# Kernel tuning notes

Measured on AMD Instinct MI355X. Metric: run time of the kernel, lower is better.

The kernel has to match this reference:

```python
import jax, jax.numpy as jnp
import jax.lax as lax
import numpy as np

# ---- Parallel3DGeometry constants ----
B, C = 1, 1
D, H, W = 64, 96, 96          # internal volume layout (z, y, x)
V, U, A = 64, 96, 90          # detector rows, detector cols, projection angles
SX = SY = SD = 1.0            # voxel size (x, y, z)
SU = SV = 1.0                 # detector spacing
NSTEPS = H + W + 2            # upper bound on voxels crossed by an XY ray
DIAG = float(np.sqrt(SX * SX + SY * SY))
EPS = 1e-12


def _t_for(p0, dp, pmin, pmax):
    # slab entry/exit parameters, matching torch _t_for (incl. parallel-ray cases)
    par = jnp.abs(dp) < EPS
    safe = jnp.where(par, 1.0, dp)
    t0 = (pmin - p0) / safe
    t1 = (pmax - p0) / safe
    lo = jnp.minimum(t0, t1)
    hi = jnp.maximum(t0, t1)
    inside = (p0 >= pmin) & (p0 <= pmax)
    lo = jnp.where(par, jnp.where(inside, -jnp.inf, jnp.inf), lo)
    hi = jnp.where(par, jnp.where(inside, jnp.inf, -jnp.inf), hi)
    return lo, hi


def _trace():
    """Vectorized Siddon XY traversal for all A*U rays.

    Returns Is, Js (int32 [A,U,NSTEPS]) voxel indices and Ws (f32 [A,U,NSTEPS])
    segment lengths (0 where the ray has exited / padded steps).
    """
    angles = jnp.linspace(0.0, np.pi, A, endpoint=False).astype(jnp.float32)
    cos_t = jnp.cos(angles)
    sin_t = jnp.sin(angles)
    u = (jnp.arange(U, dtype=jnp.float32) - (U - 1) / 2.0) * SU
    dx = jnp.broadcast_to(cos_t[:, None], (A, U)).reshape(-1)
    dy = jnp.broadcast_to(sin_t[:, None], (A, U)).reshape(-1)
    x0 = (-u[None, :] * sin_t[:, None]).reshape(-1)
    y0 = (u[None, :] * cos_t[:, None]).reshape(-1)

    x_min = -((W - 1) / 2.0) * SX; x_max = ((W - 1) / 2.0) * SX
    y_min = -((H - 1) / 2.0) * SY; y_max = ((H - 1) / 2.0) * SY
    tx0, tx1 = _t_for(x0, dx, x_min, x_max)
    ty0, ty1 = _t_for(y0, dy, y_min, y_max)
    t_entry = jnp.maximum(tx0, ty0)
    t_exit = jnp.minimum(tx1, ty1)
    alive0 = t_entry < t_exit
    te = jnp.where(alive0, t_entry, 0.0)
    tex = jnp.where(alive0, t_exit, 0.0)
    xe = x0 + te * dx
    ye = y0 + te * dy
    i0 = jnp.clip(jnp.round(xe / SX + (W - 1) / 2.0), 0, W - 1).astype(jnp.int32)
    j0 = jnp.clip(jnp.round(ye / SY + (H - 1) / 2.0), 0, H - 1).astype(jnp.int32)
    cxw = (W - 1) / 2.0 * SX
    cyh = (H - 1) / 2.0 * SY

    def body(st, _):
        i, j, x, y, t, alive = st
        valid = alive & (t < tex - EPS)
        fi = i.astype(jnp.float32)
        fj = j.astype(jnp.float32)
        xn = jnp.where(dx > 0, (fi + 0.5) * SX - cxw,
                       jnp.where(dx < 0, (fi - 0.5) * SX - cxw, jnp.inf))
        yn = jnp.where(dy > 0, (fj + 0.5) * SY - cyh,
                       jnp.where(dy < 0, (fj - 0.5) * SY - cyh, jnp.inf))
        okx = jnp.abs(dx) > EPS
        oky = jnp.abs(dy) > EPS
        tx = jnp.where(okx, (xn - x) / jnp.where(okx, dx, 1.0), jnp.inf)
        ty = jnp.where(oky, (yn - y) / jnp.where(oky, dy, 1.0), jnp.inf)
        dt = jnp.minimum(jnp.minimum(tx, ty), tex - t)
        seg = jnp.maximum(0.0, dt * DIAG / jnp.maximum(jnp.abs(dx) + jnp.abs(dy), EPS))
        w = jnp.where(valid, seg, 0.0)
        i_n = i + jnp.where(tx <= ty, jnp.where(dx > 0, 1, -1), 0)
        j_n = j + jnp.where(ty <= tx, jnp.where(dy > 0, 1, -1), 0)
        inb = (i_n >= 0) & (i_n < W) & (j_n >= 0) & (j_n < H)
        dts = jnp.where(valid, dt, 0.0)
        st2 = (jnp.where(valid, i_n, i), jnp.where(valid, j_n, j),
               x + dx * dts, y + dy * dts, t + dts, valid & inb)
        return st2, (i, j, w)

    init = (i0, j0, xe, ye, te, alive0)
    _, (Is, Js, Ws) = lax.scan(body, init, None, length=NSTEPS)
    # [NSTEPS, R] -> [A, U, NSTEPS]
    Is = Is.T.reshape(A, U, NSTEPS)
    Js = Js.T.reshape(A, U, NSTEPS)
    Ws = Ws.T.reshape(A, U, NSTEPS)
    return Is, Js, Ws


def _forward(vol):
    # model-facing [B,C,X,Y,Z] -> internal [B,C,D,H,W]
    vol_int = jnp.transpose(vol, (0, 1, 4, 3, 2))
    Is, Js, Ws = _trace()
    v_phys = (jnp.arange(V, dtype=jnp.float32) - (V - 1) / 2.0) * SV
    k = jnp.clip(jnp.round(v_phys / SD + (D - 1) / 2.0), 0, D - 1).astype(jnp.int32)
    # gather voxel values along every ray: [B,C,V,A,U,NSTEPS]
    g = vol_int[:, :, k[:, None, None, None], Js[None], Is[None]]
    out = jnp.einsum('bcvaun,aun->bcvau', g, Ws.astype(vol.dtype))
    # internal [B,C,V,A,U] (== out[b,c,a,v,u] reordered) -> model-facing [B,C,U,A,V]
    return jnp.transpose(out, (0, 1, 4, 3, 2))


def setup_inputs() -> dict:
    key = jax.random.key(0)
    vol = jax.random.normal(key, (B, C, W, H, D), dtype=jnp.float32)
    return {"vol": vol}


def reference(vol):
    return _forward(vol)
```

## Files before the change

### kernel.cpp

```cpp
#include <hip/hip_runtime.h>
#include <math.h>

namespace {
constexpr int NA = 90, NU = 96, NV = 64, NW = 96, NH = 96, ND = 64;
constexpr int NRAY   = NA * NU;
constexpr int NVOX   = NW * NH * ND;
constexpr int NENT   = 256;
constexpr int CNTMAX = 208;
constexpr int TILE   = 8;
constexpr int NBLK   = 1024;
constexpr int NEXTRA = NRAY - NBLK * TILE;
}

__device__ inline void sincos_poly(double xd, float* s, float* c)
{
    const double INV_PIO2 = 0.63661977236758134308;
    const double PIO2_HI  = 1.57079632679489655800e+00;
    const double PIO2_LO  = 6.12323399573676603587e-17;
    const double qd = rint(xd * INV_PIO2);
    const double r  = (xd - qd * PIO2_HI) - qd * PIO2_LO;
    const double z  = r * r;
    const double sp = r + (r * z) * (-1.66666666666666324348e-01 + z *
                     ( 8.33333333332248946124e-03 + z *
                     (-1.98412698298579493134e-04 + z *
                     ( 2.75573137070700676789e-06 + z *
                     (-2.50507602534068634195e-08 + z *
                       1.58969099521155010221e-10)))));
    const double cp = 1.0 + z * (-0.5 + z *
                     ( 4.16666666666666019037e-02 + z *
                     (-1.38888888888741095749e-03 + z *
                     ( 2.48015872894767294178e-05 + z *
                     (-2.75573143513906633035e-07 + z *
                     ( 2.08757232129817482790e-09 + z *
                      -1.13596475577881948265e-11))))));
    const int q = (int)qd;
    const double sv = (q == 0) ? sp : ((q == 1) ? cp : -sp);
    const double cv = (q == 0) ? cp : ((q == 1) ? -sp : -cp);
    *s = (float)sv;
    *c = (float)cv;
}

template <bool CONSUME>
__device__ __forceinline__ void do_ray(const float* __restrict__ vol,
                                       float* __restrict__ out,
                                       int2* __restrict__ myRow,
                                       const int ray, const int lane,
                                       const float4 wA, const float4 wB)
{
    const int a = ray / NU;
    const int u = ray - a * NU;

    const float EPSf = 1e-12f;
    const float INFp = __builtin_inff();
    const float DIAG = 1.41421356237309514547f;

    const float ang = (float)a * (float)(3.14159265358979323846 / 90.0);
    float dy, dx;
    sincos_poly((double)ang, &dy, &dx);
    const float uu = (float)u - 47.5f;
    const float x0 = __fmul_rn(-uu, dy);
    const float y0 = __fmul_rn( uu, dx);

    const float xmin = -47.5f, xmax = 47.5f;
    const float ymin = -47.5f, ymax = 47.5f;

    float tx0, tx1;
    {
        const bool par = fabsf(dx) < EPSf;
        const float safe = par ? 1.0f : dx;
        const float t0 = __fdiv_rn(xmin - x0, safe);
        const float t1 = __fdiv_rn(xmax - x0, safe);
        const float lo = fminf(t0, t1), hi = fmaxf(t0, t1);
        const bool inside = (x0 >= xmin) && (x0 <= xmax);
        tx0 = par ? (inside ? -INFp : INFp) : lo;
        tx1 = par ? (inside ?  INFp : -INFp) : hi;
    }
    float ty0, ty1;
    {
        const bool par = fabsf(dy) < EPSf;
        const float safe = par ? 1.0f : dy;
        const float t0 = __fdiv_rn(ymin - y0, safe);
        const float t1 = __fdiv_rn(ymax - y0, safe);
        const float lo = fminf(t0, t1), hi = fmaxf(t0, t1);
        const bool inside = (y0 >= ymin) && (y0 <= ymax);
        ty0 = par ? (inside ? -INFp : INFp) : lo;
        ty1 = par ? (inside ?  INFp : -INFp) : hi;
    }

    const float t_entry = fmaxf(tx0, ty0);
    const float t_exit  = fminf(tx1, ty1);
    const bool  alive0  = t_entry < t_exit;
    const float te  = alive0 ? t_entry : 0.0f;
    const float tex = alive0 ? t_exit  : 0.0f;

    const float xe = __fadd_rn(x0, __fmul_rn(te, dx));
    const float ye = __fadd_rn(y0, __fmul_rn(te, dy));
    const int i0 = (int)fminf(fmaxf(rintf(__fadd_rn(xe, 47.5f)), 0.0f), 95.0f);
    const int j0 = (int)fminf(fmaxf(rintf(__fadd_rn(ye, 47.5f)), 0.0f), 95.0f);

    const bool okx = fabsf(dx) > EPSf;
    const bool oky = fabsf(dy) > EPSf;
    const float inv_dx = okx ? __fdiv_rn(1.0f, dx) : 0.0f;
    const float inv_dy = oky ? __fdiv_rn(1.0f, dy) : 0.0f;
    const float wscale = __fdiv_rn(DIAG, fmaxf(fabsf(dx) + fabsf(dy), EPSf));
    const float tex_m_eps = __fadd_rn(tex, -EPSf);

    const float cx = (dx > 0.0f) ? -47.0f : -48.0f;
    const float cy = (dy > 0.0f) ? -47.0f : -48.0f;
    const float Ax = okx ? __fadd_rn(te, __fmul_rn(((float)i0 + cx) - xe, inv_dx)) : INFp;
    const float Ay = oky ? __fadd_rn(te, __fmul_rn(((float)j0 + cy) - ye, inv_dy)) : INFp;
    const float px = okx ? fabsf(inv_dx) : 0.0f;
    const float py = oky ? fabsf(inv_dy) : 0.0f;
    const int   si = (dx > 0.0f) ? 1 : -1;
    const int   sj = (dy > 0.0f) ? 1 : -1;

    const float inv_pq = __fdiv_rn(1.0f, px + py);
    const float Cc = Ay - Ax;

    int cnt = 0;
    #pragma unroll
    for (int rnd = 0; rnd < 4; ++rnd) {
        const int n = (rnd << 6) + lane;
        const float nf = (float)n;

        float kf = __fmul_rn(__fmaf_rn(nf, py, Cc), inv_pq);
        kf = fminf(fmaxf(kf, 0.0f), nf);
        int k = (int)rintf(kf);

        #pragma unroll
        for (int it = 0; it < 4; ++it) {
            const int m = n - k;
            const float Txk   = __fmaf_rn((float)k, px, Ax);
            const float Txkm1 = (k > 0) ? __fmaf_rn((float)(k - 1), px, Ax) : -INFp;
            const float Tyl   = __fmaf_rn((float)m, py, Ay);
            const float Tylm1 = (m > 0) ? __fmaf_rn((float)(m - 1), py, Ay) : -INFp;
            const bool dec = (Txkm1 > Tyl);
            const bool inc = (!dec) && (Tylm1 > Txk);
            k += inc ? 1 : (dec ? -1 : 0);
        }

        const int m = n - k;
        const float Txk   = __fmaf_rn((float)k, px, Ax);
        const float Txkm1 = (k > 0) ? __fmaf_rn((float)(k - 1), px, Ax) : -INFp;
        const float Tyl   = __fmaf_rn((float)m, py, Ay);
        const float Tylm1 = (m > 0) ? __fmaf_rn((float)(m - 1), py, Ay) : -INFp;

        const float Tn   = fminf(Txk, Tyl);
        const float prev = fmaxf(te, fmaxf(Txkm1, Tylm1));
        const float dt   = __fadd_rn(fminf(Tn, tex), -fminf(prev, tex));
        const bool active = alive0 && (prev < tex_m_eps);
        float w = __fmul_rn(fmaxf(0.0f, dt), wscale);
        w = active ? w : 0.0f;

        const int ii = min(95, max(0, i0 + ((si > 0) ? k : -k)));
        const int jj = min(95, max(0, j0 + ((sj > 0) ? m : -m)));
        int2 e;
        e.x = (ii * NH + jj) << 8;
        e.y = __float_as_int(w);
        myRow[n] = e;

        cnt += (int)__popcll(__ballot(active));
    }
    const int cap = min((cnt + 15) & ~15, CNTMAX);

    if (CONSUME) {
        asm volatile("" :: "v"(wA.x), "v"(wA.y), "v"(wA.z), "v"(wA.w),
                           "v"(wB.x), "v"(wB.y), "v"(wB.z), "v"(wB.w));
    }

    const int r   = lane >> 4;
    const int sub = lane & 15;
    const int subOff = sub << 4;

    const int2* __restrict__ eRow = myRow + r;
    const char* __restrict__ vb   = (const char*)vol;

    float4 acc[4] = {{0,0,0,0}, {0,0,0,0}, {0,0,0,0}, {0,0,0,0}};
    for (int n = 0; n < cap; n += 16) {
        const int2 e0 = eRow[n];
        const int2 e1 = eRow[n + 4];
        const int2 e2 = eRow[n + 8];
        const int2 e3 = eRow[n + 12];
        const float4 v0 = *(const float4*)(vb + (e0.x + subOff));
        const float4 v1 = *(const float4*)(vb + (e1.x + subOff));
        const float4 v2 = *(const float4*)(vb + (e2.x + subOff));
        const float4 v3 = *(const float4*)(vb + (e3.x + subOff));
        const float w0 = __int_as_float(e0.y);
        const float w1 = __int_as_float(e1.y);
        const float w2 = __int_as_float(e2.y);
        const float w3 = __int_as_float(e3.y);
        acc[0].x = fmaf(w0, v0.x, acc[0].x); acc[0].y = fmaf(w0, v0.y, acc[0].y);
        acc[0].z = fmaf(w0, v0.z, acc[0].z); acc[0].w = fmaf(w0, v0.w, acc[0].w);
        acc[1].x = fmaf(w1, v1.x, acc[1].x); acc[1].y = fmaf(w1, v1.y, acc[1].y);
        acc[1].z = fmaf(w1, v1.z, acc[1].z); acc[1].w = fmaf(w1, v1.w, acc[1].w);
        acc[2].x = fmaf(w2, v2.x, acc[2].x); acc[2].y = fmaf(w2, v2.y, acc[2].y);
        acc[2].z = fmaf(w2, v2.z, acc[2].z); acc[2].w = fmaf(w2, v2.w, acc[2].w);
        acc[3].x = fmaf(w3, v3.x, acc[3].x); acc[3].y = fmaf(w3, v3.y, acc[3].y);
        acc[3].z = fmaf(w3, v3.z, acc[3].z); acc[3].w = fmaf(w3, v3.w, acc[3].w);
    }

    float sx = (acc[0].x + acc[1].x) + (acc[2].x + acc[3].x);
    float sy = (acc[0].y + acc[1].y) + (acc[2].y + acc[3].y);
    float sz = (acc[0].z + acc[1].z) + (acc[2].z + acc[3].z);
    float sw = (acc[0].w + acc[1].w) + (acc[2].w + acc[3].w);

    sx += __shfl_xor(sx, 16, 64);  sy += __shfl_xor(sy, 16, 64);
    sz += __shfl_xor(sz, 16, 64);  sw += __shfl_xor(sw, 16, 64);
    sx += __shfl_xor(sx, 32, 64);  sy += __shfl_xor(sy, 32, 64);
    sz += __shfl_xor(sz, 32, 64);  sw += __shfl_xor(sw, 32, 64);

    if (lane < 16) {
        float4 res; res.x = sx; res.y = sy; res.z = sz; res.w = sw;
        *(float4*)(out + (u * NA + a) * NV + (sub << 2)) = res;
    }
}

__global__ __launch_bounds__(512)
void siddon_fused(const float* __restrict__ vol, float* __restrict__ out)
{
    __shared__ int2 sEnt[TILE][NENT];

    const int tid  = threadIdx.x;
    const int wid  = tid >> 6;
    const int lane = tid & 63;
    const int bid  = blockIdx.x;

    float4 wA = {0, 0, 0, 0}, wB = {0, 0, 0, 0};
    {
        const int nchunks = NVOX / 4;
        const int base = (bid >> 3) * 1152;
        const int iA = base + tid;
        const int iB = base + 512 + tid;
        const int hi = min(base + 1152, nchunks);
        if (iA < hi) wA = *(const float4*)(vol + (size_t)iA * 4);
        if (iB < hi) wB = *(const float4*)(vol + (size_t)iB * 4);
    }

    int2* __restrict__ myRow = &sEnt[wid][0];

    const int ray0 = bid * TILE + wid;
    do_ray<true>(vol, out, myRow, ray0, lane, wA, wB);

    if (bid < NEXTRA && wid == ((bid + (bid >> 8)) & 7)) {
        do_ray<false>(vol, out, myRow, NBLK * TILE + bid, lane, wA, wB);
    }
}

extern "C" void kernel_launch(void* const* d_in, const int* in_sizes, int n_in,
                              void* d_out, int out_size, void* d_ws, size_t ws_size,
                              hipStream_t stream) {
    const float* vol = (const float*)d_in[0];
    float* out = (float*)d_out;
    hipLaunchKernelGGL(siddon_fused, dim3(NBLK), dim3(512), 0, stream, vol, out);
}
```

Before: 68.44 us.

## Drop L2 prewarm loads, scalarize per-ray constants, raise launch bounds occupancy

Removes the cooperative volume prefetch, where each block read a slice of the volume into registers to warm the cache before tracing. Wave-uniform ray parameters are forced into scalar registers with readfirstlane, and the alive0 check is folded into tex_m_eps. Launch bounds now request 8 blocks per CU. The aim is lower VGPR pressure and higher occupancy, at the risk of more cold cache misses on the gather loads now that the prewarm is gone.

```diff
diff --git a/kernel.cpp b/kernel.cpp
--- a/kernel.cpp
+++ b/kernel.cpp
@@ -4,7 +4,6 @@
 namespace {
 constexpr int NA = 90, NU = 96, NV = 64, NW = 96, NH = 96, ND = 64;
 constexpr int NRAY   = NA * NU;
-constexpr int NVOX   = NW * NH * ND;
 constexpr int NENT   = 256;
 constexpr int CNTMAX = 208;
 constexpr int TILE   = 8;
@@ -40,12 +39,17 @@
     *c = (float)cv;
 }
 
-template <bool CONSUME>
+__device__ __forceinline__ float rflf(float x) {
+    return __int_as_float(__builtin_amdgcn_readfirstlane(__float_as_int(x)));
+}
+__device__ __forceinline__ int rfli(int x) {
+    return __builtin_amdgcn_readfirstlane(x);
+}
+
 __device__ __forceinline__ void do_ray(const float* __restrict__ vol,
                                        float* __restrict__ out,
                                        int2* __restrict__ myRow,
-                                       const int ray, const int lane,
-                                       const float4 wA, const float4 wB)
+                                       const int ray, const int lane)
 {
     const int a = ray / NU;
     const int u = ray - a * NU;
@@ -90,32 +94,32 @@
     const float t_entry = fmaxf(tx0, ty0);
     const float t_exit  = fminf(tx1, ty1);
     const bool  alive0  = t_entry < t_exit;
-    const float te  = alive0 ? t_entry : 0.0f;
-    const float tex = alive0 ? t_exit  : 0.0f;
+    const float te  = rflf(alive0 ? t_entry : 0.0f);
+    const float tex = rflf(alive0 ? t_exit  : 0.0f);
 
     const float xe = __fadd_rn(x0, __fmul_rn(te, dx));
     const float ye = __fadd_rn(y0, __fmul_rn(te, dy));
-    const int i0 = (int)fminf(fmaxf(rintf(__fadd_rn(xe, 47.5f)), 0.0f), 95.0f);
-    const int j0 = (int)fminf(fmaxf(rintf(__fadd_rn(ye, 47.5f)), 0.0f), 95.0f);
+    const int i0 = rfli((int)fminf(fmaxf(rintf(__fadd_rn(xe, 47.5f)), 0.0f), 95.0f));
+    const int j0 = rfli((int)fminf(fmaxf(rintf(__fadd_rn(ye, 47.5f)), 0.0f), 95.0f));
 
     const bool okx = fabsf(dx) > EPSf;
     const bool oky = fabsf(dy) > EPSf;
     const float inv_dx = okx ? __fdiv_rn(1.0f, dx) : 0.0f;
     const float inv_dy = oky ? __fdiv_rn(1.0f, dy) : 0.0f;
-    const float wscale = __fdiv_rn(DIAG, fmaxf(fabsf(dx) + fabsf(dy), EPSf));
-    const float tex_m_eps = __fadd_rn(tex, -EPSf);
+    const float wscale = rflf(__fdiv_rn(DIAG, fmaxf(fabsf(dx) + fabsf(dy), EPSf)));
+    const float tex_m_eps = rflf(__fadd_rn(tex, -EPSf));
 
     const float cx = (dx > 0.0f) ? -47.0f : -48.0f;
     const float cy = (dy > 0.0f) ? -47.0f : -48.0f;
-    const float Ax = okx ? __fadd_rn(te, __fmul_rn(((float)i0 + cx) - xe, inv_dx)) : INFp;
-    const float Ay = oky ? __fadd_rn(te, __fmul_rn(((float)j0 + cy) - ye, inv_dy)) : INFp;
-    const float px = okx ? fabsf(inv_dx) : 0.0f;
-    const float py = oky ? fabsf(inv_dy) : 0.0f;
-    const int   si = (dx > 0.0f) ? 1 : -1;
-    const int   sj = (dy > 0.0f) ? 1 : -1;
-
-    const float inv_pq = __fdiv_rn(1.0f, px + py);
-    const float Cc = Ay - Ax;
+    const float Ax = rflf(okx ? __fadd_rn(te, __fmul_rn(((float)i0 + cx) - xe, inv_dx)) : INFp);
+    const float Ay = rflf(oky ? __fadd_rn(te, __fmul_rn(((float)j0 + cy) - ye, inv_dy)) : INFp);
+    const float px = rflf(okx ? fabsf(inv_dx) : 0.0f);
+    const float py = rflf(oky ? fabsf(inv_dy) : 0.0f);
+    const int   si = rfli((dx > 0.0f) ? 1 : -1);
+    const int   sj = rfli((dy > 0.0f) ? 1 : -1);
+
+    const float inv_pq = rflf(__fdiv_rn(1.0f, px + py));
+    const float Cc = rflf(Ay - Ax);
 
     int cnt = 0;
     #pragma unroll
@@ -148,7 +152,7 @@
         const float Tn   = fminf(Txk, Tyl);
         const float prev = fmaxf(te, fmaxf(Txkm1, Tylm1));
         const float dt   = __fadd_rn(fminf(Tn, tex), -fminf(prev, tex));
-        const bool active = alive0 && (prev < tex_m_eps);
+        const bool active = (prev < tex_m_eps);
         float w = __fmul_rn(fmaxf(0.0f, dt), wscale);
         w = active ? w : 0.0f;
 
@@ -162,11 +166,6 @@
         cnt += (int)__popcll(__ballot(active));
     }
     const int cap = min((cnt + 15) & ~15, CNTMAX);
-
-    if (CONSUME) {
-        asm volatile("" :: "v"(wA.x), "v"(wA.y), "v"(wA.z), "v"(wA.w),
-                           "v"(wB.x), "v"(wB.y), "v"(wB.z), "v"(wB.w));
-    }
 
     const int r   = lane >> 4;
     const int sub = lane & 15;
@@ -215,7 +214,7 @@
     }
 }
 
-__global__ __launch_bounds__(512)
+__global__ __launch_bounds__(512, 8)
 void siddon_fused(const float* __restrict__ vol, float* __restrict__ out)
 {
     __shared__ int2 sEnt[TILE][NENT];
@@ -225,24 +224,13 @@
     const int lane = tid & 63;
     const int bid  = blockIdx.x;
 
-    float4 wA = {0, 0, 0, 0}, wB = {0, 0, 0, 0};
-    {
-        const int nchunks = NVOX / 4;
-        const int base = (bid >> 3) * 1152;
-        const int iA = base + tid;
-        const int iB = base + 512 + tid;
-        const int hi = min(base + 1152, nchunks);
-        if (iA < hi) wA = *(const float4*)(vol + (size_t)iA * 4);
-        if (iB < hi) wB = *(const float4*)(vol + (size_t)iB * 4);
-    }
-
     int2* __restrict__ myRow = &sEnt[wid][0];
 
     const int ray0 = bid * TILE + wid;
-    do_ray<true>(vol, out, myRow, ray0, lane, wA, wB);
+    do_ray(vol, out, myRow, ray0, lane);
 
     if (bid < NEXTRA && wid == ((bid + (bid >> 8)) & 7)) {
-        do_ray<false>(vol, out, myRow, NBLK * TILE + bid, lane, wA, wB);
+        do_ray(vol, out, myRow, NBLK * TILE + bid, lane);
     }
 }
 
```

Result: no change. 68.37 us (-0.1%).
